# Kernel optimization log

Measured on AMD Instinct MI355X. Metric: run time of the kernel, lower is better.

The kernel has to match this reference:

```python
import jax, jax.numpy as jnp
import numpy as np

N_HEADS = 16
N_KV_HEADS = 4
HEAD_DIM = 128


def apply_rotary_emb(x, cos, sin):
    # x: [B, S, H, D]; cos/sin: [S, D//2]
    xr = x[..., 0::2]
    xi = x[..., 1::2]
    c = cos[None, :, None, :]
    s = sin[None, :, None, :]
    out_r = xr * c - xi * s
    out_i = xr * s + xi * c
    # interleave back: [..., D//2, 2] -> [..., D]
    return jnp.stack([out_r, out_i], axis=-1).reshape(x.shape)


def setup_inputs() -> dict:
    key = jax.random.key(0)
    ks = jax.random.split(key, 7)
    B, S, D = 4, 2048, 2048
    x = jax.random.normal(ks[0], (B, S, D), dtype=jnp.float32)
    # realistic rotary tables
    inv_freq = 1.0 / (10000.0 ** (jnp.arange(0, HEAD_DIM, 2, dtype=jnp.float32) / HEAD_DIM))
    t = jnp.arange(S, dtype=jnp.float32)
    freqs = jnp.outer(t, inv_freq)  # [S, D/2]
    freqs_cos = jnp.cos(freqs)
    freqs_sin = jnp.sin(freqs)
    sc = 0.02
    wq = jax.random.normal(ks[1], (D, N_HEADS * HEAD_DIM), dtype=jnp.float32) * sc
    wk = jax.random.normal(ks[2], (D, N_KV_HEADS * HEAD_DIM), dtype=jnp.float32) * sc
    wv = jax.random.normal(ks[3], (D, N_KV_HEADS * HEAD_DIM), dtype=jnp.float32) * sc
    wo = jax.random.normal(ks[4], (N_HEADS * HEAD_DIM, D), dtype=jnp.float32) * sc
    return {"x": x, "freqs_cos": freqs_cos, "freqs_sin": freqs_sin,
            "wq": wq, "wk": wk, "wv": wv, "wo": wo}


def reference(x, freqs_cos, freqs_sin, wq, wk, wv, wo):
    B, S, D = x.shape
    n_rep = N_HEADS // N_KV_HEADS
    xq = (x @ wq).reshape(B, S, N_HEADS, HEAD_DIM)
    xk = (x @ wk).reshape(B, S, N_KV_HEADS, HEAD_DIM)
    xv = (x @ wv).reshape(B, S, N_KV_HEADS, HEAD_DIM)
    xq = apply_rotary_emb(xq, freqs_cos, freqs_sin)
    xk = apply_rotary_emb(xk, freqs_cos, freqs_sin)
    # repeat_kv (GQA): [B,S,Hkv,D] -> [B,S,Hkv*n_rep,D]
    xk = jnp.repeat(xk, n_rep, axis=2)
    xv = jnp.repeat(xv, n_rep, axis=2)
    # [B,H,S,D]
    q = xq.transpose(0, 2, 1, 3)
    k = xk.transpose(0, 2, 1, 3)
    v = xv.transpose(0, 2, 1, 3)
    scores = jnp.einsum('bhqd,bhkd->bhqk', q, k) / jnp.sqrt(jnp.float32(HEAD_DIM))
    causal = jnp.triu(jnp.ones((S, S), dtype=bool), k=1)
    scores = jnp.where(causal[None, None], -jnp.inf, scores)
    probs = jax.nn.softmax(scores, axis=-1)
    out = jnp.einsum('bhqk,bhkd->bhqd', probs, v)
    out = out.transpose(0, 2, 1, 3).reshape(B, S, N_HEADS * HEAD_DIM)
    return out @ wo
```

## Files before the change

kernel.cpp:

```cpp
#include <hip/hip_runtime.h>
#include <stdint.h>
#include <stddef.h>

#define B_ 4
#define S_ 2048
#define D_ 2048
#define NH 16
#define NKV 4
#define HD 128
#define QKV_N 3072
#define ROWS (B_*S_)

typedef unsigned short u16;
typedef __attribute__((ext_vector_type(8))) unsigned short u16x8;
typedef __attribute__((ext_vector_type(8))) __bf16 bf16x8;
typedef __attribute__((ext_vector_type(4))) float f32x4;

__device__ __forceinline__ u16 f2bf(float f) {
  unsigned u = __builtin_bit_cast(unsigned, f);
  return (u16)((u + 0x7fffu + ((u >> 16) & 1u)) >> 16);
}
__device__ __forceinline__ float bf2f(u16 h) {
  return __builtin_bit_cast(float, (unsigned)h << 16);
}
__device__ __forceinline__ f32x4 mfma16(u16x8 a, u16x8 b, f32x4 c) {
  return __builtin_amdgcn_mfma_f32_16x16x32_bf16(
      __builtin_bit_cast(bf16x8, a), __builtin_bit_cast(bf16x8, b), c, 0, 0, 0);
}
__device__ __forceinline__ void gld16(const void* g, void* l) {
  __builtin_amdgcn_global_load_lds(
      (const __attribute__((address_space(1))) void*)g,
      (__attribute__((address_space(3))) void*)l, 16, 0, 0);
}

__global__ __launch_bounds__(256) void k_cast_x(const float* __restrict__ x, u16* __restrict__ xb) {
  int i = blockIdx.x * 256 + threadIdx.x;
  float4 v = ((const float4*)x)[i];
  union { u16 u[4]; uint2 p; } o;
  o.u[0] = f2bf(v.x); o.u[1] = f2bf(v.y); o.u[2] = f2bf(v.z); o.u[3] = f2bf(v.w);
  ((uint2*)xb)[i] = o.p;
}

__global__ __launch_bounds__(256) void k_wt(const float* __restrict__ w, u16* __restrict__ wt, int K, int N) {
  __shared__ float tile[32][33];
  int kb = blockIdx.y * 32, nb = blockIdx.x * 32;
  int tx = threadIdx.x, ty = threadIdx.y;
#pragma unroll
  for (int j = 0; j < 32; j += 8)
    tile[ty + j][tx] = w[(size_t)(kb + ty + j) * N + nb + tx];
  __syncthreads();
#pragma unroll
  for (int j = 0; j < 32; j += 8)
    wt[(size_t)(nb + ty + j) * K + kb + tx] = f2bf(tile[tx][ty + j]);
}


#define STG_A(KK, SS) do {                                                   \
    _Pragma("unroll") for (int j_ = 0; j_ < 2; ++j_)                         \
      gld16(Ag + (size_t)(j_ * 128 + r0) * 2048 + (KK) + coff,               \
            As + (SS) * 8192 + j_ * 4096 + stl0);                            \
  } while (0)
#define STG_B(KK, SS) do {                                                   \
    _Pragma("unroll") for (int j_ = 0; j_ < BN / 128; ++j_)                  \
      gld16(Bg + (size_t)(j_ * 128 + r0) * 2048 + (KK) + coff,               \
            Bs + (SS) * (BN * 32) + j_ * 4096 + stl0);                       \
  } while (0)

#define VMW() do {                                                           \
    if constexpr (BN == 256) asm volatile("s_waitcnt vmcnt(8)" ::: "memory");\
    else                     asm volatile("s_waitcnt vmcnt(10)" ::: "memory");\
  } while (0)

#define PHASE(RS, MB, RB, SS, SK, SA, VM) do {                               \
    const u16* Ap_ = As + (RS) * 8192;                                       \
    _Pragma("unroll") for (int i_ = 0; i_ < 4; ++i_)                         \
      af[i_] = *(const u16x8*)(Ap_ + arow0 + ((MB) + i_) * 512);             \
    if (RB) {                                                                \
      const u16* Bp_ = Bs + (RS) * (BN * 32);                                \
      _Pragma("unroll") for (int i_ = 0; i_ < BN / 64; ++i_)                 \
        bf[i_] = *(const u16x8*)(Bp_ + brow0 + i_ * 512);                    \
    }                                                                        \
    if (SA) STG_A(SK, SS); else STG_B(SK, SS);                               \
    asm volatile("s_barrier" ::: "memory");                                  \
    asm volatile("s_waitcnt lgkmcnt(0)" ::: "memory");                       \
    __builtin_amdgcn_sched_barrier(0);                                       \
    __builtin_amdgcn_s_setprio(1);                                           \
    _Pragma("unroll") for (int i_ = 0; i_ < 4; ++i_)                         \
      _Pragma("unroll") for (int n_ = 0; n_ < BN / 64; ++n_)                 \
        acc[(MB) + i_][n_] = mfma16(af[i_], bf[n_], acc[(MB) + i_][n_]);     \
    __builtin_amdgcn_s_setprio(0);                                           \
    __builtin_amdgcn_sched_barrier(0);                                       \
    if (VM) VMW();                                                           \
    asm volatile("s_barrier" ::: "memory");                                  \
  } while (0)

template<int NT, int BN, bool F32OUT>
__global__ __launch_bounds__(512, 2) void k_gemm(const u16* __restrict__ A, const u16* __restrict__ Bt,
                                                 void* __restrict__ C) {
  __shared__ u16 As[4 * 8192];
  __shared__ u16 Bs[4 * (BN * 32)];
  int id = blockIdx.x;
  int nwg = gridDim.x;
  id = (id & 7) * (nwg >> 3) + (id >> 3);
  const int gx = NT / BN;
  int mb = (id / gx) * 256, nb = (id % gx) * BN;

  int t = threadIdx.x;
  int l = t & 63, L16 = l & 15, quad = l >> 4;
  int w = t >> 6, wm = w >> 2, wn = w & 3;
  const int schunk = 8 * (quad ^ ((L16 >> 1) & 3));
  const int arow0 = (wm * 128 + L16) * 32 + schunk;
  const int brow0 = (wn * (BN / 4) + L16) * 32 + schunk;
  const int r0 = t >> 2;
  const int coff = 8 * ((t & 3) ^ ((r0 >> 1) & 3));
  const int stl0 = (t & 448) * 8;

  const u16* Ag = A + (size_t)mb * 2048;
  const u16* Bg = Bt + (size_t)nb * 2048;
  u16x8 af[4], bf[BN / 64];
  f32x4 acc[8][BN / 64] = {};

  STG_A(0, 0);  STG_B(0, 0);
  STG_A(32, 1); STG_B(32, 1);
  STG_A(64, 2); STG_B(64, 2);
  VMW();
  asm volatile("s_barrier" ::: "memory");

#pragma unroll 2
  for (int tt = 0; tt < 32; ++tt) {
    int rs0 = (2 * tt) & 3, rs1 = (2 * tt + 1) & 3;
    int ss1 = (2 * tt + 3) & 3;
    int k1n = ((tt + 1) & 31) * 64 + 32;
    int k0n = ((tt + 2) & 31) * 64;
    PHASE(rs0, 0, true,  ss1, k1n, true,  false);
    PHASE(rs0, 4, false, ss1, k1n, false, true);
    PHASE(rs1, 0, true,  rs0, k0n, true,  false);
    PHASE(rs1, 4, false, rs0, k0n, false, true);
  }
  asm volatile("s_waitcnt vmcnt(0)" ::: "memory");

#pragma unroll
  for (int m = 0; m < 8; ++m)
#pragma unroll
    for (int n = 0; n < BN / 64; ++n)
#pragma unroll
      for (int r = 0; r < 4; ++r) {
        int row = mb + wm * 128 + m * 16 + quad * 4 + r;
        int col = nb + wn * (BN / 4) + n * 16 + L16;
        if constexpr (F32OUT)
          ((float*)C)[(size_t)row * NT + col] = acc[m][n][r];
        else
          ((u16*)C)[(size_t)row * NT + col] = f2bf(acc[m][n][r]);
      }
}

__global__ __launch_bounds__(256) void k_rope(const u16* __restrict__ qkv, const float* __restrict__ fc,
                                              const float* __restrict__ fs, u16* __restrict__ Q,
                                              u16* __restrict__ Kk) {
  const float SC = 0.1275174214f;
  int row = blockIdx.x;
  int b = row >> 11, s = row & 2047;
  int t = threadIdx.x;
#pragma unroll
  for (int j = 0; j < 5; ++j) {
    int p = t + j * 256;
    int i = p & 63;
    float c = fc[s * 64 + i], sn = fs[s * 64 + i];
    if (p < 1024) {
      int h = p >> 6;
      unsigned pr = *(const unsigned*)(qkv + (size_t)row * QKV_N + h * 128 + 2 * i);
      float xr = bf2f((u16)(pr & 0xffff)), xi = bf2f((u16)(pr >> 16));
      size_t o = (((size_t)(b * NH + h) * S_) + s) * HD + 2 * i;
      unsigned out = (unsigned)f2bf((xr * c - xi * sn) * SC) |
                     ((unsigned)f2bf((xr * sn + xi * c) * SC) << 16);
      *(unsigned*)(Q + o) = out;
    } else {
      int kh = (p - 1024) >> 6;
      unsigned pr = *(const unsigned*)(qkv + (size_t)row * QKV_N + 2048 + kh * 128 + 2 * i);
      float xr = bf2f((u16)(pr & 0xffff)), xi = bf2f((u16)(pr >> 16));
      size_t o = (((size_t)(b * NKV + kh) * S_) + s) * HD + 2 * i;
      unsigned out = (unsigned)f2bf(xr * c - xi * sn) | ((unsigned)f2bf(xr * sn + xi * c) << 16);
      *(unsigned*)(Kk + o) = out;
    }
  }
}

__global__ __launch_bounds__(256) void k_vt(const u16* __restrict__ qkv, u16* __restrict__ Vt) {
  __shared__ u16 tile[64 * 128];
  int blk = blockIdx.x;
  int sb = blk & 31, kh = (blk >> 5) & 3, b = blk >> 7;
  int t = threadIdx.x;
  int s0 = sb * 64;
#pragma unroll
  for (int i = 0; i < 4; ++i) {
    int lin = i * 256 + t;
    int row = lin >> 4, c = lin & 15;
    u16x8 v = *(const u16x8*)(qkv + (size_t)(b * S_ + s0 + row) * QKV_N + 2560 + kh * HD + c * 8);
    *(u16x8*)(tile + row * 128 + ((c ^ (row & 15)) * 8)) = v;
  }
  __syncthreads();
#pragma unroll
  for (int i = 0; i < 2; ++i) {
    int u = i * 256 + t;
    int p = u >> 3, o = u & 7;
    u16 lo[8], hi[8];
#pragma unroll
    for (int j = 0; j < 8; ++j) {
      int s = o * 8 + j;
      int cs = (p >> 2) ^ (s & 15);
      unsigned v = *(const unsigned*)(tile + s * 128 + cs * 8 + (p & 3) * 2);
      lo[j] = (u16)(v & 0xffff); hi[j] = (u16)(v >> 16);
    }
    size_t ob = ((size_t)(b * NKV + kh) * HD + 2 * p) * S_ + s0 + o * 8;
    *(u16x8*)(Vt + ob)      = *(u16x8*)lo;
    *(u16x8*)(Vt + ob + S_) = *(u16x8*)hi;
  }
}

__global__ __launch_bounds__(256) void k_attn(const u16* __restrict__ Q, const u16* __restrict__ Kg,
                                              const u16* __restrict__ Vt, u16* __restrict__ O) {
  int bx = blockIdx.x;
  int bh = bx >> 3, pr = bx & 7;
  int b = bh >> 4, h = bh & 15, kh = h >> 2;
  int t = threadIdx.x;
  int w = t >> 6, l = t & 63, L = l & 15, quad = l >> 4;

  __shared__ u16 Ks[64 * 128];
  __shared__ u16 Vs[128 * 64];
  __shared__ u16 Ps[4][32 * 72];
  u16* Pw = &Ps[w][0];

  const u16* Qh = Q  + ((size_t)(b * NH  + h ) * S_) * HD;
  const u16* Kh = Kg + ((size_t)(b * NKV + kh) * S_) * HD;
  const u16* Vh = Vt + ((size_t)(b * NKV + kh) * HD) * S_;

  u16x8 ones;
#pragma unroll
  for (int i = 0; i < 8; ++i) ones[i] = 0x3F80;

  int koff[4], voff[2];
#pragma unroll
  for (int kk = 0; kk < 4; ++kk) koff[kk] = 128 * L + 8 * ((4 * kk + quad) ^ (L & 7));
#pragma unroll
  for (int kc = 0; kc < 2; ++kc) voff[kc] = 64 * L + 8 * ((4 * kc + quad) ^ (L & 7));
  const int pread  = 72 * L + 8 * quad;
  const int pwrite = 72 * L + 4 * quad;

  int kgo[4], vgo[4], klo[4], vlo[4];
#pragma unroll
  for (int i = 0; i < 4; ++i) {
    int lin = i * 256 + t;
    int row = lin >> 4, c = lin & 15;
    kgo[i] = row * HD + ((c ^ (row & 7)) * 8);
    int d = lin >> 3, c2 = lin & 7;
    vgo[i] = d * S_ + ((c2 ^ (d & 7)) * 8);
    klo[i] = (i * 256 + (t & 192)) * 8;
    vlo[i] = (i * 256 + (t & 192)) * 8;
  }

#pragma unroll 1
  for (int half = 0; half < 2; ++half) {
    int qb = half ? (15 - pr) : pr;
    int q0 = qb * 128 + w * 32;

    u16x8 qf[2][4];
#pragma unroll
    for (int m = 0; m < 2; ++m)
#pragma unroll
      for (int kk = 0; kk < 4; ++kk)
        qf[m][kk] = *(const u16x8*)(Qh + (size_t)(q0 + m * 16 + L) * HD + kk * 32 + quad * 8);

    f32x4 acc[2][9] = {};
    int ktiles = 2 * qb + 2;
#pragma unroll 1
    for (int kt = 0; kt < ktiles; ++kt) {
      int kbase = kt * 64;
      __syncthreads();
      const u16* Kt = Kh + (size_t)kbase * HD;
      const u16* Vg = Vh + kbase;
#pragma unroll
      for (int i = 0; i < 4; ++i) gld16(Kt + kgo[i], Ks + klo[i]);
#pragma unroll
      for (int i = 0; i < 4; ++i) gld16(Vg + vgo[i], Vs + vlo[i]);
      __syncthreads();
      if (kbase > q0 + 31) continue;

      bool needMask = (kbase + 63 > q0);
#pragma unroll
      for (int n = 0; n < 4; ++n) {
        f32x4 s0v = {}, s1v = {};
#pragma unroll
        for (int kk = 0; kk < 4; ++kk) {
          u16x8 kf = *(const u16x8*)(Ks + koff[kk] + 2048 * n);
          s0v = mfma16(kf, qf[0][kk], s0v);
          s1v = mfma16(kf, qf[1][kk], s1v);
        }
#pragma unroll
        for (int m = 0; m < 2; ++m) {
          f32x4 sv = m ? s1v : s0v;
          int qrow = q0 + m * 16 + L;
          unsigned eu[4];
#pragma unroll
          for (int r = 0; r < 4; ++r) {
            float e = exp2f(sv[r]);
            if (needMask) {
              int key = kbase + n * 16 + quad * 4 + r;
              e = (key <= qrow) ? e : 0.0f;
            }
            eu[r] = __builtin_bit_cast(unsigned, e);
          }
          uint2 pk;
          pk.x = __builtin_amdgcn_perm(eu[1], eu[0], 0x07060302u);
          pk.y = __builtin_amdgcn_perm(eu[3], eu[2], 0x07060302u);
          *(uint2*)(Pw + pwrite + 1152 * m + 16 * n) = pk;
        }
      }
#pragma unroll
      for (int kc = 0; kc < 2; ++kc) {
        u16x8 pf0 = *(const u16x8*)(Pw + pread + 32 * kc);
        u16x8 pf1 = *(const u16x8*)(Pw + pread + 1152 + 32 * kc);
#pragma unroll
        for (int nt = 0; nt < 8; ++nt) {
          u16x8 vf = *(const u16x8*)(Vs + voff[kc] + 1024 * nt);
          acc[0][nt] = mfma16(pf0, vf, acc[0][nt]);
          acc[1][nt] = mfma16(pf1, vf, acc[1][nt]);
        }
        acc[0][8] = mfma16(pf0, ones, acc[0][8]);
        acc[1][8] = mfma16(pf1, ones, acc[1][8]);
      }
    }
#pragma unroll
    for (int m = 0; m < 2; ++m)
#pragma unroll
      for (int r = 0; r < 4; ++r) {
        float inv = 1.0f / acc[m][8][r];
        int qrow = q0 + m * 16 + quad * 4 + r;
#pragma unroll
        for (int nt = 0; nt < 8; ++nt) {
          int col = h * HD + nt * 16 + L;
          O[(size_t)(b * S_ + qrow) * D_ + col] = f2bf(acc[m][nt][r] * inv);
        }
      }
  }
}

extern "C" void kernel_launch(void* const* d_in, const int* in_sizes, int n_in,
                              void* d_out, int out_size, void* d_ws, size_t ws_size,
                              hipStream_t stream) {
  const float* x  = (const float*)d_in[0];
  const float* fc = (const float*)d_in[1];
  const float* fs = (const float*)d_in[2];
  const float* wq = (const float*)d_in[3];
  const float* wk = (const float*)d_in[4];
  const float* wv = (const float*)d_in[5];
  const float* wo = (const float*)d_in[6];
  float* out = (float*)d_out;

  u16* p = (u16*)d_ws;
  u16* xb    = p; p += (size_t)ROWS * D_;
  u16* wqkvT = p; p += (size_t)QKV_N * D_;
  u16* woT   = p; p += (size_t)D_ * D_;
  u16* qkv   = p; p += (size_t)ROWS * QKV_N;
  u16* Qr    = p; p += (size_t)ROWS * (NH * HD);
  u16* Kr    = p; p += (size_t)ROWS * (NKV * HD);
  u16* Vtr   = p; p += (size_t)ROWS * (NKV * HD);
  u16* AO    = p; p += (size_t)ROWS * D_;

  k_cast_x<<<dim3(ROWS * D_ / 1024), dim3(256), 0, stream>>>(x, xb);
  k_wt<<<dim3(64, 64), dim3(32, 8), 0, stream>>>(wq, wqkvT, 2048, 2048);
  k_wt<<<dim3(16, 64), dim3(32, 8), 0, stream>>>(wk, wqkvT + (size_t)2048 * 2048, 2048, 512);
  k_wt<<<dim3(16, 64), dim3(32, 8), 0, stream>>>(wv, wqkvT + (size_t)2560 * 2048, 2048, 512);
  k_wt<<<dim3(64, 64), dim3(32, 8), 0, stream>>>(wo, woT, 2048, 2048);
  k_gemm<QKV_N, 384, false><<<dim3((QKV_N / 384) * (ROWS / 256)), dim3(512), 0, stream>>>(xb, wqkvT, qkv);
  k_rope<<<dim3(ROWS), dim3(256), 0, stream>>>(qkv, fc, fs, Qr, Kr);
  k_vt<<<dim3(B_ * NKV * (S_ / 64)), dim3(256), 0, stream>>>(qkv, Vtr);
  k_attn<<<dim3(64 * 8), dim3(256), 0, stream>>>(Qr, Kr, Vtr, AO);
  k_gemm<D_, 256, true><<<dim3((D_ / 256) * (ROWS / 256)), dim3(512), 0, stream>>>(AO, woT, out);
}
```

Baseline: 446.4 us.

## Double-buffer K/V tiles in attention with 32-key tiles and async prefetch

Result: faster. 422.0 us (-5.5%).

```diff
diff --git a/kernel.cpp b/kernel.cpp
--- a/kernel.cpp
+++ b/kernel.cpp
@@ -16,6 +16,12 @@
 typedef __attribute__((ext_vector_type(8))) __bf16 bf16x8;
 typedef __attribute__((ext_vector_type(4))) float f32x4;
 
+#if __has_builtin(__builtin_amdgcn_exp2f)
+#define EXP2F(x) __builtin_amdgcn_exp2f(x)
+#else
+#define EXP2F(x) exp2f(x)
+#endif
+
 __device__ __forceinline__ u16 f2bf(float f) {
   unsigned u = __builtin_bit_cast(unsigned, f);
   return (u16)((u + 0x7fffu + ((u >> 16) & 1u)) >> 16);
@@ -53,7 +59,6 @@
   for (int j = 0; j < 32; j += 8)
     wt[(size_t)(nb + ty + j) * K + kb + tx] = f2bf(tile[tx][ty + j]);
 }
-
 
 #define STG_A(KK, SS) do {                                                   \
     _Pragma("unroll") for (int j_ = 0; j_ < 2; ++j_)                         \
@@ -225,9 +230,9 @@
   int t = threadIdx.x;
   int w = t >> 6, l = t & 63, L = l & 15, quad = l >> 4;
 
-  __shared__ u16 Ks[64 * 128];
-  __shared__ u16 Vs[128 * 64];
-  __shared__ u16 Ps[4][32 * 72];
+  __shared__ u16 Ks[2][32 * 128];
+  __shared__ u16 Vs[2][128 * 32];
+  __shared__ u16 Ps[4][32 * 40];
   u16* Pw = &Ps[w][0];
 
   const u16* Qh = Q  + ((size_t)(b * NH  + h ) * S_) * HD;
@@ -238,24 +243,22 @@
 #pragma unroll
   for (int i = 0; i < 8; ++i) ones[i] = 0x3F80;
 
-  int koff[4], voff[2];
+  int koff[4];
 #pragma unroll
   for (int kk = 0; kk < 4; ++kk) koff[kk] = 128 * L + 8 * ((4 * kk + quad) ^ (L & 7));
-#pragma unroll
-  for (int kc = 0; kc < 2; ++kc) voff[kc] = 64 * L + 8 * ((4 * kc + quad) ^ (L & 7));
-  const int pread  = 72 * L + 8 * quad;
-  const int pwrite = 72 * L + 4 * quad;
-
-  int kgo[4], vgo[4], klo[4], vlo[4];
-#pragma unroll
-  for (int i = 0; i < 4; ++i) {
+  const int voff   = 32 * L + 8 * (quad ^ ((L >> 1) & 3));
+  const int pread  = 40 * L + 8 * quad;
+  const int pwrite = 40 * L + 4 * quad;
+
+  int kgo[2], vgo[2], slo[2];
+#pragma unroll
+  for (int i = 0; i < 2; ++i) {
     int lin = i * 256 + t;
-    int row = lin >> 4, c = lin & 15;
-    kgo[i] = row * HD + ((c ^ (row & 7)) * 8);
-    int d = lin >> 3, c2 = lin & 7;
-    vgo[i] = d * S_ + ((c2 ^ (d & 7)) * 8);
-    klo[i] = (i * 256 + (t & 192)) * 8;
-    vlo[i] = (i * 256 + (t & 192)) * 8;
+    int kr = lin >> 4, kc = lin & 15;
+    kgo[i] = kr * HD + ((kc ^ (kr & 7)) * 8);
+    int vd = lin >> 2, vc = lin & 3;
+    vgo[i] = vd * S_ + ((vc ^ ((vd >> 1) & 3)) * 8);
+    slo[i] = (i * 256 + (t & 192)) * 8;
   }
 
 #pragma unroll 1
@@ -269,29 +272,43 @@
 #pragma unroll
       for (int kk = 0; kk < 4; ++kk)
         qf[m][kk] = *(const u16x8*)(Qh + (size_t)(q0 + m * 16 + L) * HD + kk * 32 + quad * 8);
+    asm volatile("s_waitcnt vmcnt(0)" ::: "memory");
+    __builtin_amdgcn_sched_barrier(0);
 
     f32x4 acc[2][9] = {};
-    int ktiles = 2 * qb + 2;
-#pragma unroll 1
+    int ktiles = 4 * qb + 4;
+#pragma unroll
+    for (int i = 0; i < 2; ++i) gld16(Kh + kgo[i], &Ks[0][0] + slo[i]);
+#pragma unroll
+    for (int i = 0; i < 2; ++i) gld16(Vh + vgo[i], &Vs[0][0] + slo[i]);
+
+#pragma unroll 2
     for (int kt = 0; kt < ktiles; ++kt) {
-      int kbase = kt * 64;
-      __syncthreads();
-      const u16* Kt = Kh + (size_t)kbase * HD;
-      const u16* Vg = Vh + kbase;
-#pragma unroll
-      for (int i = 0; i < 4; ++i) gld16(Kt + kgo[i], Ks + klo[i]);
-#pragma unroll
-      for (int i = 0; i < 4; ++i) gld16(Vg + vgo[i], Vs + vlo[i]);
-      __syncthreads();
+      int kbase = kt * 32;
+      int cur = kt & 1;
+      asm volatile("s_barrier" ::: "memory");
+      int kb2 = (32 * (kt + 1)) & (S_ - 1);
+      const u16* Kt = Kh + (size_t)kb2 * HD;
+      const u16* Vg = Vh + kb2;
+      u16* Kn = &Ks[cur ^ 1][0];
+      u16* Vn = &Vs[cur ^ 1][0];
+#pragma unroll
+      for (int i = 0; i < 2; ++i) gld16(Kt + kgo[i], Kn + slo[i]);
+#pragma unroll
+      for (int i = 0; i < 2; ++i) gld16(Vg + vgo[i], Vn + slo[i]);
+      asm volatile("s_waitcnt vmcnt(4)" ::: "memory");
+      asm volatile("s_barrier" ::: "memory");
       if (kbase > q0 + 31) continue;
 
-      bool needMask = (kbase + 63 > q0);
-#pragma unroll
-      for (int n = 0; n < 4; ++n) {
+      bool needMask = (kbase + 31 > q0);
+      const u16* Kc = &Ks[cur][0];
+      const u16* Vc = &Vs[cur][0];
+#pragma unroll
+      for (int n = 0; n < 2; ++n) {
         f32x4 s0v = {}, s1v = {};
 #pragma unroll
         for (int kk = 0; kk < 4; ++kk) {
-          u16x8 kf = *(const u16x8*)(Ks + koff[kk] + 2048 * n);
+          u16x8 kf = *(const u16x8*)(Kc + koff[kk] + 2048 * n);
           s0v = mfma16(kf, qf[0][kk], s0v);
           s1v = mfma16(kf, qf[1][kk], s1v);
         }
@@ -302,7 +319,7 @@
           unsigned eu[4];
 #pragma unroll
           for (int r = 0; r < 4; ++r) {
-            float e = exp2f(sv[r]);
+            float e = EXP2F(sv[r]);
             if (needMask) {
               int key = kbase + n * 16 + quad * 4 + r;
               e = (key <= qrow) ? e : 0.0f;
@@ -312,23 +329,23 @@
           uint2 pk;
           pk.x = __builtin_amdgcn_perm(eu[1], eu[0], 0x07060302u);
           pk.y = __builtin_amdgcn_perm(eu[3], eu[2], 0x07060302u);
-          *(uint2*)(Pw + pwrite + 1152 * m + 16 * n) = pk;
+          *(uint2*)(Pw + pwrite + 640 * m + 16 * n) = pk;
         }
       }
-#pragma unroll
-      for (int kc = 0; kc < 2; ++kc) {
-        u16x8 pf0 = *(const u16x8*)(Pw + pread + 32 * kc);
-        u16x8 pf1 = *(const u16x8*)(Pw + pread + 1152 + 32 * kc);
-#pragma unroll
-        for (int nt = 0; nt < 8; ++nt) {
-          u16x8 vf = *(const u16x8*)(Vs + voff[kc] + 1024 * nt);
-          acc[0][nt] = mfma16(pf0, vf, acc[0][nt]);
-          acc[1][nt] = mfma16(pf1, vf, acc[1][nt]);
-        }
-        acc[0][8] = mfma16(pf0, ones, acc[0][8]);
-        acc[1][8] = mfma16(pf1, ones, acc[1][8]);
+      u16x8 pf0 = *(const u16x8*)(Pw + pread);
+      u16x8 pf1 = *(const u16x8*)(Pw + pread + 640);
+#pragma unroll
+      for (int nt = 0; nt < 8; ++nt) {
+        u16x8 vf = *(const u16x8*)(Vc + voff + 512 * nt);
+        acc[0][nt] = mfma16(pf0, vf, acc[0][nt]);
+        acc[1][nt] = mfma16(pf1, vf, acc[1][nt]);
       }
+      acc[0][8] = mfma16(pf0, ones, acc[0][8]);
+      acc[1][8] = mfma16(pf1, ones, acc[1][8]);
     }
+    asm volatile("s_waitcnt vmcnt(0)" ::: "memory");
+    asm volatile("s_barrier" ::: "memory");
+
 #pragma unroll
     for (int m = 0; m < 2; ++m)
 #pragma unroll
```
